# Kernel tuning notes

Measured on AMD Instinct MI355X. Metric: run time of the kernel, lower is better.

Reference implementation:

```python
import jax, jax.numpy as jnp
import numpy as np


def setup_inputs() -> dict:
    key = jax.random.key(0)
    k0, k1, k2, k3 = jax.random.split(key, 4)
    B, M, H, K, OUT = 256, 64, 64, 128, 256
    x0 = jax.random.normal(k0, (B, M, K), dtype=jnp.float32)
    xl = jax.random.normal(k1, (B, H, K), dtype=jnp.float32)
    # Conv1d(in_channels=M*H, out_channels=OUT, kernel_size=1) params
    fan_in = M * H  # kernel_size=1
    bound = 1.0 / np.sqrt(fan_in)
    W = jax.random.uniform(k2, (OUT, M * H, 1), dtype=jnp.float32, minval=-bound, maxval=bound)
    b = jax.random.uniform(k3, (OUT,), dtype=jnp.float32, minval=-bound, maxval=bound)
    return {"x0": x0, "xl": xl, "k": K, "W": W, "b": b}


def reference(x0, xl, k, W, b):
    # x0: [B, m, k_emb], xl: [B, h, k_emb]
    # Fused equivalent of the per-column loop: for each embedding column i,
    # matmul(xl[:,:,i:i+1], x0[:,:,i:i+1]^T) -> [B,h,m]; stacked over k -> [B,h,m,k]
    fmap = jnp.einsum('bhk,bmk->bhmk', xl, x0)
    B = x0.shape[0]
    h, m = xl.shape[1], x0.shape[1]
    fmap = fmap.reshape(B, h * m, k)  # [B, h*m, k]
    # 1x1 Conv1d == GEMM over channel dim
    out = jnp.einsum('bck,oc->bok', fmap, W[:, :, 0]) + b[None, :, None]
    return out
```

## Files before the change

### kernel.cpp

```cpp
#include <hip/hip_runtime.h>
#include <hip/hip_bf16.h>
#include <stdint.h>


typedef __attribute__((ext_vector_type(8))) short short8;
typedef __attribute__((ext_vector_type(4))) float f32x4;

#define B_SZ   256
#define K_SZ   128
#define OUT_SZ 256
#define C_SZ   4096
#define NCHUNK 64

__device__ __forceinline__ uint32_t pack_bf16(float a, float b) {
    __hip_bfloat162 h2 = __float22bfloat162_rn(make_float2(a, b));
    union { __hip_bfloat162 h; uint32_t u; } v;
    v.h = h2;
    return v.u;
}

__device__ __forceinline__ void load_lds_16(const void* g, void* l) {
    __builtin_amdgcn_global_load_lds(
        (const __attribute__((address_space(1))) unsigned int*)g,
        (__attribute__((address_space(3))) unsigned int*)l,
        16, 0, 0);
}

__global__ void convert_W_tiled(const float* __restrict__ W, short* __restrict__ Wb) {
    int t = blockIdx.x * blockDim.x + threadIdx.x;
    int lane = t & 63;
    int cb   = (t >> 6) & 127;
    int got  = t >> 13;
    int o = got * 16 + (lane & 15);
    int c = cb * 32 + (lane >> 4) * 8;
    const float* p = W + (size_t)o * C_SZ + c;
    float4 w0 = *(const float4*)p;
    float4 w1 = *(const float4*)(p + 4);
    union { short8 s; uint32_t u[4]; } cc;
    cc.u[0] = pack_bf16(w0.x, w0.y);
    cc.u[1] = pack_bf16(w0.z, w0.w);
    cc.u[2] = pack_bf16(w1.x, w1.y);
    cc.u[3] = pack_bf16(w1.z, w1.w);
    *(short8*)(Wb + (size_t)t * 8) = cc.s;
}

template<bool USE_WS>
__global__ __launch_bounds__(512, 4)
void cin_main(const float* __restrict__ x0, const float* __restrict__ xl,
              const float* __restrict__ Wf, const short* __restrict__ Wb,
              const float* __restrict__ bias, float* __restrict__ out) {
    __shared__ float xlf[64 * 128];
    __shared__ short Wlds[2 * 8192];

    const int b     = blockIdx.y;
    const int ohalf = blockIdx.x;
    const int tid   = threadIdx.x;
    const int lane  = tid & 63;
    const int wave  = tid >> 6;
    const int wo    = wave >> 1;
    const int wk    = wave & 1;
    const int rl    = lane & 15;
    const int kg    = lane >> 4;

    {
        const float4* src = (const float4*)(xl + (size_t)b * (64 * K_SZ));
        float4* dst = (float4*)xlf;
#pragma unroll
        for (int i = 0; i < 4; ++i)
            dst[tid * 4 + i] = src[tid * 4 + i];
    }

    union { short8 s; uint32_t u[4]; } x0p[2][4];
    {
        const float* x0b = x0 + (size_t)b * (64 * K_SZ);
        const int col0 = wk * 64 + rl;
#pragma unroll
        for (int ks = 0; ks < 2; ++ks)
#pragma unroll
            for (int nt = 0; nt < 4; ++nt)
#pragma unroll
                for (int j = 0; j < 4; ++j) {
                    const int r0 = ks * 32 + kg * 8 + 2 * j;
                    const int cc = col0 + nt * 16;
                    x0p[ks][nt].u[j] = pack_bf16(x0b[r0 * K_SZ + cc],
                                                 x0b[(r0 + 1) * K_SZ + cc]);
                }
    }

    const short* wsrc = Wb + ((size_t)(ohalf * 8 + wave) * 128) * 512 + lane * 8;
    const float* wfrow = Wf + (size_t)((ohalf * 8 + wave) * 16 + rl) * C_SZ + kg * 8;
    short* wdst0 = Wlds + (wave * 2 + 0) * 512;
    short* wdst1 = Wlds + (wave * 2 + 1) * 512;
    short* wown  = Wlds + (wave * 2) * 512 + lane * 8;

    auto stage = [&](int buf, int h) {
        if (USE_WS) {
            const short* s = wsrc + (size_t)h * 1024;
            load_lds_16(s,       wdst0 + buf * 8192);
            load_lds_16(s + 512, wdst1 + buf * 8192);
        } else {
#pragma unroll
            for (int cbl = 0; cbl < 2; ++cbl) {
                const float* p = wfrow + (2 * h + cbl) * 32;
                float4 w0 = *(const float4*)p;
                float4 w1 = *(const float4*)(p + 4);
                union { short8 s; uint32_t u[4]; } cc;
                cc.u[0] = pack_bf16(w0.x, w0.y);
                cc.u[1] = pack_bf16(w0.z, w0.w);
                cc.u[2] = pack_bf16(w1.x, w1.y);
                cc.u[3] = pack_bf16(w1.z, w1.w);
                *(short8*)(wown + buf * 8192 + cbl * 512) = cc.s;
            }
        }
    };

    f32x4 acc[2][4];
#pragma unroll
    for (int ot = 0; ot < 2; ++ot)
#pragma unroll
        for (int nt = 0; nt < 4; ++nt)
            acc[ot][nt] = (f32x4){0.f, 0.f, 0.f, 0.f};
    const f32x4 kz = (f32x4){0.f, 0.f, 0.f, 0.f};

    stage(0, 0);
    __syncthreads();

    const float* xlrow = xlf + wk * 64 + rl;
    int cur = 0;

    for (int h = 0; h < NCHUNK; ++h) {
        if (h < NCHUNK - 1) stage(cur ^ 1, h + 1);

        float xlv[4];
#pragma unroll
        for (int nt = 0; nt < 4; ++nt)
            xlv[nt] = xlrow[h * K_SZ + nt * 16];

#pragma unroll
        for (int ot = 0; ot < 2; ++ot) {
            const short* wb = Wlds + cur * 8192 + ((wo * 2 + ot) * 2) * 512 + lane * 8;
            const short8 af0 = *(const short8*)(wb);
            const short8 af1 = *(const short8*)(wb + 512);
#pragma unroll
            for (int nt = 0; nt < 4; ++nt) {
                f32x4 g = __builtin_amdgcn_mfma_f32_16x16x32_bf16(af0, x0p[0][nt].s, kz, 0, 0, 0);
                g = __builtin_amdgcn_mfma_f32_16x16x32_bf16(af1, x0p[1][nt].s, g, 0, 0, 0);
#pragma unroll
                for (int r = 0; r < 4; ++r)
                    acc[ot][nt][r] += xlv[nt] * g[r];
            }
        }
        __syncthreads();
        cur ^= 1;
    }

    float* outb = out + (size_t)b * (OUT_SZ * K_SZ);
#pragma unroll
    for (int ot = 0; ot < 2; ++ot) {
        const int o0 = ohalf * 128 + wo * 32 + ot * 16 + kg * 4;
#pragma unroll
        for (int r = 0; r < 4; ++r) {
            const float bv = bias[o0 + r];
#pragma unroll
            for (int nt = 0; nt < 4; ++nt)
                outb[(o0 + r) * K_SZ + wk * 64 + nt * 16 + rl] = acc[ot][nt][r] + bv;
        }
    }
}

extern "C" void kernel_launch(void* const* d_in, const int* in_sizes, int n_in,
                              void* d_out, int out_size, void* d_ws, size_t ws_size,
                              hipStream_t stream) {
    const float* x0   = (const float*)d_in[0];
    const float* xl   = (const float*)d_in[1];
    const float* W    = (const float*)d_in[3];
    const float* bias = (const float*)d_in[4];
    float* out = (float*)d_out;

    const size_t w_bytes = (size_t)OUT_SZ * C_SZ * sizeof(short);
    short* Wb = (short*)d_ws;

    if (ws_size >= w_bytes) {
        convert_W_tiled<<<dim3(512), dim3(256), 0, stream>>>(W, Wb);
        cin_main<true><<<dim3(2, B_SZ), dim3(512), 0, stream>>>(x0, xl, W, Wb, bias, out);
    } else {
        cin_main<false><<<dim3(2, B_SZ), dim3(512), 0, stream>>>(x0, xl, W, Wb, bias, out);
    }
}
```

Measured before the change: 77.57 us.

## Use 32x32x16 MFMA, one block per batch covering all outputs, 4-stage W pipeline

After: 92.33 us. 19.0% more time.

```diff
diff --git a/kernel.cpp b/kernel.cpp
--- a/kernel.cpp
+++ b/kernel.cpp
@@ -3,14 +3,14 @@
 #include <stdint.h>
 
 
-typedef __attribute__((ext_vector_type(8))) short short8;
-typedef __attribute__((ext_vector_type(4))) float f32x4;
+typedef __attribute__((ext_vector_type(8)))  short short8;
+typedef __attribute__((ext_vector_type(16))) float f32x16;
 
 #define B_SZ   256
 #define K_SZ   128
 #define OUT_SZ 256
 #define C_SZ   4096
-#define NCHUNK 64
+#define NH     64
 
 __device__ __forceinline__ uint32_t pack_bf16(float a, float b) {
     __hip_bfloat162 h2 = __float22bfloat162_rn(make_float2(a, b));
@@ -19,6 +19,12 @@
     return v.u;
 }
 
+__device__ __forceinline__ float bf2f(short s) {
+    union { uint32_t u; float f; } v;
+    v.u = ((uint32_t)(uint16_t)s) << 16;
+    return v.f;
+}
+
 __device__ __forceinline__ void load_lds_16(const void* g, void* l) {
     __builtin_amdgcn_global_load_lds(
         (const __attribute__((address_space(1))) unsigned int*)g,
@@ -29,10 +35,11 @@
 __global__ void convert_W_tiled(const float* __restrict__ W, short* __restrict__ Wb) {
     int t = blockIdx.x * blockDim.x + threadIdx.x;
     int lane = t & 63;
-    int cb   = (t >> 6) & 127;
-    int got  = t >> 13;
-    int o = got * 16 + (lane & 15);
-    int c = cb * 32 + (lane >> 4) * 8;
+    int sub  = t >> 6;
+    int cb16 = sub & 255;
+    int got  = sub >> 8;
+    int o = got * 32 + (lane & 31);
+    int c = cb16 * 16 + (lane >> 5) * 8;
     const float* p = W + (size_t)o * C_SZ + c;
     float4 w0 = *(const float4*)p;
     float4 w1 = *(const float4*)(p + 4);
@@ -45,63 +52,63 @@
 }
 
 template<bool USE_WS>
-__global__ __launch_bounds__(512, 4)
+__global__ __launch_bounds__(512, 2)
 void cin_main(const float* __restrict__ x0, const float* __restrict__ xl,
               const float* __restrict__ Wf, const short* __restrict__ Wb,
               const float* __restrict__ bias, float* __restrict__ out) {
-    __shared__ float xlf[64 * 128];
-    __shared__ short Wlds[2 * 8192];
-
-    const int b     = blockIdx.y;
-    const int ohalf = blockIdx.x;
-    const int tid   = threadIdx.x;
-    const int lane  = tid & 63;
-    const int wave  = tid >> 6;
-    const int wo    = wave >> 1;
-    const int wk    = wave & 1;
-    const int rl    = lane & 15;
-    const int kg    = lane >> 4;
+    __shared__ short Wlds[4 * 16384];
+    __shared__ short xls[NH * K_SZ];
+
+    const int b    = blockIdx.x;
+    const int tid  = threadIdx.x;
+    const int lane = tid & 63;
+    const int wave = tid >> 6;
+    const int l31  = lane & 31;
+    const int hi   = lane >> 5;
 
     {
-        const float4* src = (const float4*)(xl + (size_t)b * (64 * K_SZ));
-        float4* dst = (float4*)xlf;
-#pragma unroll
-        for (int i = 0; i < 4; ++i)
-            dst[tid * 4 + i] = src[tid * 4 + i];
-    }
-
-    union { short8 s; uint32_t u[4]; } x0p[2][4];
+        const float4* src = (const float4*)(xl + (size_t)b * (NH * K_SZ));
+        float4 v[4];
+#pragma unroll
+        for (int i = 0; i < 4; ++i) v[i] = src[tid * 4 + i];
+        uint32_t* dst = (uint32_t*)&xls[tid * 16];
+#pragma unroll
+        for (int i = 0; i < 4; ++i) {
+            dst[2 * i]     = pack_bf16(v[i].x, v[i].y);
+            dst[2 * i + 1] = pack_bf16(v[i].z, v[i].w);
+        }
+    }
+
+    union { short8 s; uint32_t u[4]; } x0p[4][4];
     {
         const float* x0b = x0 + (size_t)b * (64 * K_SZ);
-        const int col0 = wk * 64 + rl;
-#pragma unroll
-        for (int ks = 0; ks < 2; ++ks)
+#pragma unroll
+        for (int s = 0; s < 4; ++s)
 #pragma unroll
             for (int nt = 0; nt < 4; ++nt)
 #pragma unroll
-                for (int j = 0; j < 4; ++j) {
-                    const int r0 = ks * 32 + kg * 8 + 2 * j;
-                    const int cc = col0 + nt * 16;
-                    x0p[ks][nt].u[j] = pack_bf16(x0b[r0 * K_SZ + cc],
-                                                 x0b[(r0 + 1) * K_SZ + cc]);
+                for (int t2 = 0; t2 < 4; ++t2) {
+                    const int m0 = s * 16 + hi * 8 + 2 * t2;
+                    const int cc = nt * 32 + l31;
+                    x0p[s][nt].u[t2] = pack_bf16(x0b[m0 * K_SZ + cc],
+                                                 x0b[(m0 + 1) * K_SZ + cc]);
                 }
     }
 
-    const short* wsrc = Wb + ((size_t)(ohalf * 8 + wave) * 128) * 512 + lane * 8;
-    const float* wfrow = Wf + (size_t)((ohalf * 8 + wave) * 16 + rl) * C_SZ + kg * 8;
-    short* wdst0 = Wlds + (wave * 2 + 0) * 512;
-    short* wdst1 = Wlds + (wave * 2 + 1) * 512;
-    short* wown  = Wlds + (wave * 2) * 512 + lane * 8;
+    const short* wsrc = Wb + ((size_t)wave * 256) * 512 + lane * 8;
+    const float* wfrow = Wf + (size_t)(wave * 32 + l31) * C_SZ + hi * 8;
 
     auto stage = [&](int buf, int h) {
+        short* d = Wlds + buf * 16384 + wave * 2048;
         if (USE_WS) {
-            const short* s = wsrc + (size_t)h * 1024;
-            load_lds_16(s,       wdst0 + buf * 8192);
-            load_lds_16(s + 512, wdst1 + buf * 8192);
+            const short* s0 = wsrc + (size_t)(4 * h) * 512;
+#pragma unroll
+            for (int cbl = 0; cbl < 4; ++cbl)
+                load_lds_16(s0 + cbl * 512, d + cbl * 512);
         } else {
 #pragma unroll
-            for (int cbl = 0; cbl < 2; ++cbl) {
-                const float* p = wfrow + (2 * h + cbl) * 32;
+            for (int cbl = 0; cbl < 4; ++cbl) {
+                const float* p = wfrow + h * 64 + cbl * 16;
                 float4 w0 = *(const float4*)p;
                 float4 w1 = *(const float4*)(p + 4);
                 union { short8 s; uint32_t u[4]; } cc;
@@ -109,61 +116,70 @@
                 cc.u[1] = pack_bf16(w0.z, w0.w);
                 cc.u[2] = pack_bf16(w1.x, w1.y);
                 cc.u[3] = pack_bf16(w1.z, w1.w);
-                *(short8*)(wown + buf * 8192 + cbl * 512) = cc.s;
+                *(short8*)(d + cbl * 512 + lane * 8) = cc.s;
             }
         }
     };
 
-    f32x4 acc[2][4];
-#pragma unroll
-    for (int ot = 0; ot < 2; ++ot)
+    f32x16 acc[4];
+#pragma unroll
+    for (int nt = 0; nt < 4; ++nt)
+#pragma unroll
+        for (int r = 0; r < 16; ++r) acc[nt][r] = 0.f;
+    f32x16 kz;
+#pragma unroll
+    for (int r = 0; r < 16; ++r) kz[r] = 0.f;
+
+    __syncthreads();
+    stage(0, 0);
+    stage(1, 1);
+    stage(2, 2);
+
+    for (int h = 0; h < NH; ++h) {
+        if (!USE_WS) asm volatile("s_waitcnt lgkmcnt(0)" ::: "memory");
+        asm volatile("s_waitcnt vmcnt(8)" ::: "memory");
+        __builtin_amdgcn_s_barrier();
+
+        stage((h + 3) & 3, (h + 3) & (NH - 1));
+
+        const short* wb2 = Wlds + (h & 3) * 16384 + wave * 2048 + lane * 8;
+        const short8 af0 = *(const short8*)(wb2);
+        const short8 af1 = *(const short8*)(wb2 + 512);
+        const short8 af2 = *(const short8*)(wb2 + 1024);
+        const short8 af3 = *(const short8*)(wb2 + 1536);
+
+        float xlv[4];
 #pragma unroll
         for (int nt = 0; nt < 4; ++nt)
-            acc[ot][nt] = (f32x4){0.f, 0.f, 0.f, 0.f};
-    const f32x4 kz = (f32x4){0.f, 0.f, 0.f, 0.f};
-
-    stage(0, 0);
-    __syncthreads();
-
-    const float* xlrow = xlf + wk * 64 + rl;
-    int cur = 0;
-
-    for (int h = 0; h < NCHUNK; ++h) {
-        if (h < NCHUNK - 1) stage(cur ^ 1, h + 1);
-
-        float xlv[4];
-#pragma unroll
-        for (int nt = 0; nt < 4; ++nt)
-            xlv[nt] = xlrow[h * K_SZ + nt * 16];
-
-#pragma unroll
-        for (int ot = 0; ot < 2; ++ot) {
-            const short* wb = Wlds + cur * 8192 + ((wo * 2 + ot) * 2) * 512 + lane * 8;
-            const short8 af0 = *(const short8*)(wb);
-            const short8 af1 = *(const short8*)(wb + 512);
-#pragma unroll
-            for (int nt = 0; nt < 4; ++nt) {
-                f32x4 g = __builtin_amdgcn_mfma_f32_16x16x32_bf16(af0, x0p[0][nt].s, kz, 0, 0, 0);
-                g = __builtin_amdgcn_mfma_f32_16x16x32_bf16(af1, x0p[1][nt].s, g, 0, 0, 0);
-#pragma unroll
-                for (int r = 0; r < 4; ++r)
-                    acc[ot][nt][r] += xlv[nt] * g[r];
-            }
-        }
-        __syncthreads();
-        cur ^= 1;
-    }
+            xlv[nt] = bf2f(xls[h * K_SZ + nt * 32 + l31]);
+
+        __builtin_amdgcn_s_setprio(1);
+#pragma unroll
+        for (int nt = 0; nt < 4; ++nt) {
+            f32x16 g = __builtin_amdgcn_mfma_f32_32x32x16_bf16(af0, x0p[0][nt].s, kz, 0, 0, 0);
+            g = __builtin_amdgcn_mfma_f32_32x32x16_bf16(af1, x0p[1][nt].s, g, 0, 0, 0);
+            g = __builtin_amdgcn_mfma_f32_32x32x16_bf16(af2, x0p[2][nt].s, g, 0, 0, 0);
+            g = __builtin_amdgcn_mfma_f32_32x32x16_bf16(af3, x0p[3][nt].s, g, 0, 0, 0);
+#pragma unroll
+            for (int r = 0; r < 16; ++r)
+                acc[nt][r] += xlv[nt] * g[r];
+        }
+        __builtin_amdgcn_s_setprio(0);
+    }
+
+    float bv[16];
+#pragma unroll
+    for (int r = 0; r < 16; ++r)
+        bv[r] = bias[wave * 32 + (r & 3) + 8 * (r >> 2) + 4 * hi];
 
     float* outb = out + (size_t)b * (OUT_SZ * K_SZ);
 #pragma unroll
-    for (int ot = 0; ot < 2; ++ot) {
-        const int o0 = ohalf * 128 + wo * 32 + ot * 16 + kg * 4;
-#pragma unroll
-        for (int r = 0; r < 4; ++r) {
-            const float bv = bias[o0 + r];
-#pragma unroll
-            for (int nt = 0; nt < 4; ++nt)
-                outb[(o0 + r) * K_SZ + wk * 64 + nt * 16 + rl] = acc[ot][nt][r] + bv;
+    for (int nt = 0; nt < 4; ++nt) {
+        const int kcol = nt * 32 + l31;
+#pragma unroll
+        for (int r = 0; r < 16; ++r) {
+            const int orow = wave * 32 + (r & 3) + 8 * (r >> 2) + 4 * hi;
+            outb[orow * K_SZ + kcol] = acc[nt][r] + bv[r];
         }
     }
 }
@@ -182,8 +198,8 @@
 
     if (ws_size >= w_bytes) {
         convert_W_tiled<<<dim3(512), dim3(256), 0, stream>>>(W, Wb);
-        cin_main<true><<<dim3(2, B_SZ), dim3(512), 0, stream>>>(x0, xl, W, Wb, bias, out);
+        cin_main<true><<<dim3(B_SZ), dim3(512), 0, stream>>>(x0, xl, W, Wb, bias, out);
     } else {
-        cin_main<false><<<dim3(2, B_SZ), dim3(512), 0, stream>>>(x0, xl, W, Wb, bias, out);
-    }
-}
+        cin_main<false><<<dim3(B_SZ), dim3(512), 0, stream>>>(x0, xl, W, Wb, bias, out);
+    }
+}
```
